# Kernel tuning notes

Hardware: AMD Instinct MI355X
Metric: run time of the kernel (lower is better)

## Reference

```python
import jax, jax.numpy as jnp
import numpy as np

B, S, DIM = 8, 4096, 512
G, V = 2, 320            # num_groups, num_vars
CVD = 256                # codevector_dim
D = CVD // G             # per-group codevector dim = 128
TAU = 2.0                # gumbel temperature


def setup_inputs() -> dict:
    key = jax.random.key(0)
    k1, k2, k3, k4 = jax.random.split(key, 4)
    hidden_states = jax.random.normal(k1, (B, S, DIM), dtype=jnp.float32)
    # weight_proj: Linear(dim -> G*V)
    W = jax.random.normal(k2, (DIM, G * V), dtype=jnp.float32) * 0.02
    b = jnp.zeros((G * V,), dtype=jnp.float32)
    # codebook: torch init is uniform(0,1) on [1, G*V, D]; store as [G*V, D]
    codevectors = jax.random.uniform(k3, (G * V, D), dtype=jnp.float32)
    # standard Gumbel(0,1) noise, one row per (token, group)
    u = jax.random.uniform(k4, (B * S * G, V), dtype=jnp.float32,
                           minval=1e-6, maxval=1.0 - 1e-6)
    gumbels = -jnp.log(-jnp.log(u))
    return {"hidden_states": hidden_states, "W": W, "b": b,
            "codevectors": codevectors, "gumbels": gumbels}


def reference(hidden_states, W, b, codevectors, gumbels):
    Bc, Sc, _ = hidden_states.shape
    T = Bc * Sc
    # weight projection -> logits over codebook entries
    logits = hidden_states @ W + b                      # [B, S, G*V]
    flat = logits.reshape(T * G, V)                     # [T*G, V]

    # gumbel_softmax(hard=True) with straight-through estimator
    y_soft = jax.nn.softmax((flat + gumbels) / TAU, axis=-1)
    hard = jax.nn.one_hot(jnp.argmax(y_soft, axis=-1), V, dtype=y_soft.dtype)
    codevector_probs = hard + y_soft - jax.lax.stop_gradient(y_soft)

    # soft distribution (no gumbel noise, no temperature) per torch code
    codevector_dist = jax.nn.softmax(flat.reshape(T, G, V), axis=-1)

    # one-hot weighted sum over codebook = per-group contraction
    cb = codevectors.reshape(G, V, D)                   # [G, V, D]
    out = jnp.einsum('tgv,gvd->tgd',
                     codevector_probs.reshape(T, G, V), cb)
    out = out.reshape(Bc, Sc, G * D)                    # [B, S, codevector_dim]
    return (out, codevector_dist)
```

## Files before the change

kernel.cpp:

```cpp
#include <hip/hip_runtime.h>

#define Tcnt 32768
#define Gn   2
#define Vn   320
#define Dn   128
#define DIMK 512
#define GV   640
#define RB   64

typedef __attribute__((ext_vector_type(8))) short bf16x8;
typedef __attribute__((ext_vector_type(4))) ushort u16x4;
typedef __attribute__((ext_vector_type(4))) float f32x4;

__device__ inline ushort f2bf(float x) {
    unsigned u = __float_as_uint(x);
    return (ushort)((u + 0x7fffu + ((u >> 16) & 1u)) >> 16);
}

#define AS1(p) ((const __attribute__((address_space(1))) void*)(p))
#define AS3(p) ((__attribute__((address_space(3))) void*)(p))

__global__ __launch_bounds__(256) void prep_wt(
    const float* __restrict__ W, ushort* __restrict__ Wt)
{
    __shared__ ushort Ls[64][72];
    int t = blockIdx.x;
    int n0 = (t % 10) * 64, k0 = (t / 10) * 64;
    int ln = threadIdx.x & 63, kq = threadIdx.x >> 6;
    #pragma unroll
    for (int kk = 0; kk < 16; ++kk) {
        int k = kq * 16 + kk;
        Ls[k][ln] = f2bf(W[(size_t)(k0 + k) * GV + n0 + ln]);
    }
    __syncthreads();
    #pragma unroll
    for (int nn = 0; nn < 16; ++nn) {
        int n = kq * 16 + nn;
        Wt[(size_t)(n0 + n) * DIMK + k0 + ln] = Ls[ln][n];
    }
}

__global__ __launch_bounds__(512, 4) void fused_vq_kernel(
    const float*  __restrict__ hs,
    const ushort* __restrict__ Wt,
    const float*  __restrict__ W,
    const float*  __restrict__ bias,
    const float*  __restrict__ gum,
    const float*  __restrict__ cv,
    float* __restrict__ out,
    float* __restrict__ dist)
{
    __shared__ ushort As[2][RB * 32];
    __shared__ ushort Bs[2][Vn * 32];
    __shared__ float4 part[RB][2];
    __shared__ int    s_cnt[RB];
    __shared__ int    s_col[RB][8];
    __shared__ float  s_s[RB][8];
    __shared__ float  s_gm[RB][8];
    __shared__ int    s_bidx[RB];
    __shared__ float  s_mxs[RB];

    const int tid = threadIdx.x, w = tid >> 6, lane = tid & 63;
    const int Q = lane >> 4, c16 = lane & 15;
    const int wm = (w >> 1) * 16, wn = (w & 1) * 160, half = w & 1;

    const int bid = blockIdx.x;
    const int swz = (bid & 7) * 128 + (bid >> 3);
    const int g = swz & 1;
    const size_t t0 = (size_t)(swz >> 1) * RB;

    if (tid < RB) s_cnt[tid] = 0;

    const int arow_s = tid >> 3, pc = tid & 7;
    const int lq = (pc >> 1) ^ ((arow_s >> 1) & 3);
    const int lc = lq * 2 + (pc & 1);
    const float* asrc = hs + (t0 + arow_s) * DIMK + lc * 4;
    const ushort* wtg = Wt + (size_t)g * Vn * DIMK;

    auto stageB = [&](int buf, int k0) {
        #pragma unroll
        for (int i2 = 0; i2 < 2; ++i2) {
            int s = i2 * 512 + tid;
            int n = s >> 2, pq = s & 3, lqq = pq ^ ((n >> 1) & 3);
            __builtin_amdgcn_global_load_lds(
                AS1(wtg + (size_t)n * DIMK + k0 + lqq * 8),
                AS3(&Bs[buf][s * 8]), 16, 0, 0);
        }
        if (w < 4) {
            int s = 1024 + tid;
            int n = s >> 2, pq = s & 3, lqq = pq ^ ((n >> 1) & 3);
            __builtin_amdgcn_global_load_lds(
                AS1(wtg + (size_t)n * DIMK + k0 + lqq * 8),
                AS3(&Bs[buf][s * 8]), 16, 0, 0);
        }
    };
    auto writeA = [&](int buf, float4 v) {
        u16x4 o;
        o[0] = f2bf(v.x); o[1] = f2bf(v.y); o[2] = f2bf(v.z); o[3] = f2bf(v.w);
        *(u16x4*)&As[buf][tid * 4] = o;
    };

    float4 areg0 = *(const float4*)(asrc);
    stageB(0, 0);
    float4 areg1 = *(const float4*)(asrc + 32);
    writeA(0, areg0);
    __syncthreads();

    f32x4 acc[10];
    #pragma unroll
    for (int j = 0; j < 10; ++j) acc[j] = (f32x4){0.f, 0.f, 0.f, 0.f};

    #pragma unroll
    for (int ks = 0; ks < 16; ++ks) {
        if (ks + 2 < 16) {
            if ((ks & 1) == 0) areg0 = *(const float4*)(asrc + (ks + 2) * 32);
            else               areg1 = *(const float4*)(asrc + (ks + 2) * 32);
        }
        if (ks + 1 < 16) stageB((ks + 1) & 1, (ks + 1) * 32);

        const ushort* Ab = As[ks & 1];
        const ushort* Bb = Bs[ks & 1];
        const int ar = wm + c16;
        bf16x8 af = *(const bf16x8*)&Ab[(ar * 4 + (Q ^ ((ar >> 1) & 3))) * 8];
        #pragma unroll
        for (int j = 0; j < 10; ++j) {
            int n = wn + j * 16 + c16;
            bf16x8 bv = *(const bf16x8*)&Bb[(n * 4 + (Q ^ ((n >> 1) & 3))) * 8];
            acc[j] = __builtin_amdgcn_mfma_f32_16x16x32_bf16(af, bv, acc[j], 0, 0, 0);
        }
        if (ks + 1 < 16) writeA((ks + 1) & 1, ((ks + 1) & 1) ? areg1 : areg0);
        __syncthreads();
    }

    #pragma unroll
    for (int j = 0; j < 10; ++j) {
        float bb = bias[g * Vn + wn + j * 16 + c16];
        acc[j][0] += bb; acc[j][1] += bb; acc[j][2] += bb; acc[j][3] += bb;
    }

    const float MARGIN = 0.0625f;

    #pragma unroll
    for (int qr = 0; qr < 4; ++qr) {
        int row = wm + Q * 4 + qr;
        size_t r2 = (t0 + row) * 2 + g;
        const float* gr = gum + r2 * Vn + wn;
        float sv[10];
        float mxl = -1e30f, mxs = -1e30f; int bi = 0;
        #pragma unroll
        for (int j = 0; j < 10; ++j) {
            float lg = acc[j][qr];
            float gu = gr[j * 16 + c16];
            float s = lg + gu; sv[j] = s;
            mxl = fmaxf(mxl, lg);
            if (s > mxs) { mxs = s; bi = wn + j * 16 + c16; }
        }
        #pragma unroll
        for (int off = 1; off < 16; off <<= 1) {
            mxl = fmaxf(mxl, __shfl_xor(mxl, off));
            float os = __shfl_xor(mxs, off); int ob = __shfl_xor(bi, off);
            if (os > mxs || (os == mxs && ob < bi)) { mxs = os; bi = ob; }
        }
        float sum = 0.f;
        #pragma unroll
        for (int j = 0; j < 10; ++j) sum += __expf(acc[j][qr] - mxl);
        #pragma unroll
        for (int off = 1; off < 16; off <<= 1) sum += __shfl_xor(sum, off);

        float thr = mxs - MARGIN;
        #pragma unroll
        for (int j = 0; j < 10; ++j) {
            if (sv[j] >= thr) {
                int pos = atomicAdd(&s_cnt[row], 1);
                if (pos < 8) {
                    s_col[row][pos] = wn + j * 16 + c16;
                    s_s[row][pos]   = sv[j];
                    s_gm[row][pos]  = sv[j] - acc[j][qr];
                }
            }
        }
        if (c16 == 0)
            part[row][half] = (float4){mxl, sum, mxs, __int_as_float(bi)};
    }
    __syncthreads();

    #pragma unroll
    for (int qr = 0; qr < 4; ++qr) {
        int row = wm + Q * 4 + qr;
        size_t r2 = (t0 + row) * 2 + g;
        float4 mine = part[row][half];
        float4 oth  = part[row][half ^ 1];
        float mxl_f = fmaxf(mine.x, oth.x);
        float sum_f = mine.y * __expf(mine.x - mxl_f) + oth.y * __expf(oth.x - mxl_f);
        float inv = 1.0f / sum_f;
        float* dr = dist + r2 * Vn + wn;
        #pragma unroll
        for (int j = 0; j < 10; ++j)
            dr[j * 16 + c16] = __expf(acc[j][qr] - mxl_f) * inv;
        if (half == 0 && c16 == 0) {
            float ms = mine.z; int mi = __float_as_int(mine.w);
            float os = oth.z;  int oi = __float_as_int(oth.w);
            if (os > ms || (os == ms && oi < mi)) { ms = os; mi = oi; }
            s_mxs[row] = ms; s_bidx[row] = mi;
        }
    }
    __syncthreads();

    for (int ui = 0; ui < 8; ++ui) {
        int u = w * 8 + ui;
        int c = s_cnt[u]; if (c > 8) c = 8;
        float thr = s_mxs[u] - MARGIN;
        int nf = 0;
        for (int j = 0; j < c; ++j) nf += (s_s[u][j] >= thr) ? 1 : 0;
        if (nf > 1) {
            size_t t = t0 + u;
            const float* hr = hs + t * DIMK;
            float4 h0 = *(const float4*)(hr + lane * 8);
            float4 h1 = *(const float4*)(hr + lane * 8 + 4);
            float hv[8] = {h0.x, h0.y, h0.z, h0.w, h1.x, h1.y, h1.z, h1.w};
            float best = -1e30f; int bv2 = 1 << 30;
            for (int j = 0; j < c; ++j) {
                if (s_s[u][j] < thr) continue;
                int v = s_col[u][j];
                int gcol = g * Vn + v;
                const float* wc = W + gcol;
                float p = 0.f;
                #pragma unroll
                for (int i = 0; i < 8; ++i)
                    p = fmaf(hv[i], wc[(size_t)(lane * 8 + i) * GV], p);
                #pragma unroll
                for (int off = 1; off < 64; off <<= 1) p += __shfl_xor(p, off);
                float se = p + bias[gcol] + s_gm[u][j];
                if (se > best || (se == best && v < bv2)) { best = se; bv2 = v; }
            }
            if (lane == 0) s_bidx[u] = bv2;
        }
    }
    __syncthreads();

    for (int ui = 0; ui < 8; ++ui) {
        int u = w * 8 + ui;
        size_t t = t0 + u;
        int b = s_bidx[u];
        const float2* cvr = (const float2*)(cv + ((size_t)(g * Vn + b)) * Dn);
        float2 val = cvr[lane];
        *(float2*)(out + t * (Gn * Dn) + g * Dn + lane * 2) = val;
    }
}

extern "C" void kernel_launch(void* const* d_in, const int* in_sizes, int n_in,
                              void* d_out, int out_size, void* d_ws, size_t ws_size,
                              hipStream_t stream) {
    const float* hs  = (const float*)d_in[0];
    const float* W   = (const float*)d_in[1];
    const float* b   = (const float*)d_in[2];
    const float* cv  = (const float*)d_in[3];
    const float* gum = (const float*)d_in[4];

    float* out  = (float*)d_out;
    float* dist = out + (size_t)Tcnt * (Gn * Dn);
    ushort* Wt  = (ushort*)d_ws;

    prep_wt<<<80, 256, 0, stream>>>(W, Wt);
    fused_vq_kernel<<<(Tcnt / RB) * Gn, 512, 0, stream>>>(hs, Wt, W, b, gum, cv, out, dist);
}
```

Before: 95.80 us.

## Transpose logits through shared memory for row-per-wave softmax and argmax epilogue

Accumulated logits are written to a shared-memory tile (unioned with the GEMM staging buffers) in two halves, so that each wave handles whole rows with lanes spanning the vocabulary. This gives coalesced gumbel loads and dist stores, full-wave reductions, and removes the cross-wave partial-merge pass and its extra barrier. Candidate collection for exact refinement now runs only when more than one column falls inside the margin, which drops the later threshold re-check. The cost is extra LDS traffic plus barriers for the transpose, and a two-phase serialization in which half the waves sit idle while the other half write their tile.

```diff
diff --git a/kernel.cpp b/kernel.cpp
--- a/kernel.cpp
+++ b/kernel.cpp
@@ -50,19 +50,18 @@
     float* __restrict__ out,
     float* __restrict__ dist)
 {
-    __shared__ ushort As[2][RB * 32];
-    __shared__ ushort Bs[2][Vn * 32];
-    __shared__ float4 part[RB][2];
+    __shared__ union SMem {
+        struct { ushort As[2][RB * 32]; ushort Bs[2][Vn * 32]; } gm;
+        float Ls[32][324];
+    } U;
     __shared__ int    s_cnt[RB];
     __shared__ int    s_col[RB][8];
-    __shared__ float  s_s[RB][8];
     __shared__ float  s_gm[RB][8];
     __shared__ int    s_bidx[RB];
-    __shared__ float  s_mxs[RB];
 
     const int tid = threadIdx.x, w = tid >> 6, lane = tid & 63;
     const int Q = lane >> 4, c16 = lane & 15;
-    const int wm = (w >> 1) * 16, wn = (w & 1) * 160, half = w & 1;
+    const int wm = (w >> 1) * 16, wn = (w & 1) * 160;
 
     const int bid = blockIdx.x;
     const int swz = (bid & 7) * 128 + (bid >> 3);
@@ -84,20 +83,20 @@
             int n = s >> 2, pq = s & 3, lqq = pq ^ ((n >> 1) & 3);
             __builtin_amdgcn_global_load_lds(
                 AS1(wtg + (size_t)n * DIMK + k0 + lqq * 8),
-                AS3(&Bs[buf][s * 8]), 16, 0, 0);
+                AS3(&U.gm.Bs[buf][s * 8]), 16, 0, 0);
         }
         if (w < 4) {
             int s = 1024 + tid;
             int n = s >> 2, pq = s & 3, lqq = pq ^ ((n >> 1) & 3);
             __builtin_amdgcn_global_load_lds(
                 AS1(wtg + (size_t)n * DIMK + k0 + lqq * 8),
-                AS3(&Bs[buf][s * 8]), 16, 0, 0);
+                AS3(&U.gm.Bs[buf][s * 8]), 16, 0, 0);
         }
     };
     auto writeA = [&](int buf, float4 v) {
         u16x4 o;
         o[0] = f2bf(v.x); o[1] = f2bf(v.y); o[2] = f2bf(v.z); o[3] = f2bf(v.w);
-        *(u16x4*)&As[buf][tid * 4] = o;
+        *(u16x4*)&U.gm.As[buf][tid * 4] = o;
     };
 
     float4 areg0 = *(const float4*)(asrc);
@@ -118,8 +117,8 @@
         }
         if (ks + 1 < 16) stageB((ks + 1) & 1, (ks + 1) * 32);
 
-        const ushort* Ab = As[ks & 1];
-        const ushort* Bb = Bs[ks & 1];
+        const ushort* Ab = U.gm.As[ks & 1];
+        const ushort* Bb = U.gm.Bs[ks & 1];
         const int ar = wm + c16;
         bf16x8 af = *(const bf16x8*)&Ab[(ar * 4 + (Q ^ ((ar >> 1) & 3))) * 8];
         #pragma unroll
@@ -141,78 +140,78 @@
     const float MARGIN = 0.0625f;
 
     #pragma unroll
-    for (int qr = 0; qr < 4; ++qr) {
-        int row = wm + Q * 4 + qr;
-        size_t r2 = (t0 + row) * 2 + g;
-        const float* gr = gum + r2 * Vn + wn;
-        float sv[10];
-        float mxl = -1e30f, mxs = -1e30f; int bi = 0;
-        #pragma unroll
-        for (int j = 0; j < 10; ++j) {
-            float lg = acc[j][qr];
-            float gu = gr[j * 16 + c16];
-            float s = lg + gu; sv[j] = s;
-            mxl = fmaxf(mxl, lg);
-            if (s > mxs) { mxs = s; bi = wn + j * 16 + c16; }
-        }
-        #pragma unroll
-        for (int off = 1; off < 16; off <<= 1) {
-            mxl = fmaxf(mxl, __shfl_xor(mxl, off));
-            float os = __shfl_xor(mxs, off); int ob = __shfl_xor(bi, off);
-            if (os > mxs || (os == mxs && ob < bi)) { mxs = os; bi = ob; }
-        }
-        float sum = 0.f;
-        #pragma unroll
-        for (int j = 0; j < 10; ++j) sum += __expf(acc[j][qr] - mxl);
-        #pragma unroll
-        for (int off = 1; off < 16; off <<= 1) sum += __shfl_xor(sum, off);
-
-        float thr = mxs - MARGIN;
-        #pragma unroll
-        for (int j = 0; j < 10; ++j) {
-            if (sv[j] >= thr) {
-                int pos = atomicAdd(&s_cnt[row], 1);
-                if (pos < 8) {
-                    s_col[row][pos] = wn + j * 16 + c16;
-                    s_s[row][pos]   = sv[j];
-                    s_gm[row][pos]  = sv[j] - acc[j][qr];
+    for (int grp = 0; grp < 2; ++grp) {
+        __syncthreads();
+        if ((w >> 2) == grp) {
+            #pragma unroll
+            for (int qr = 0; qr < 4; ++qr) {
+                int lrow = (wm - grp * 32) + Q * 4 + qr;
+                #pragma unroll
+                for (int j = 0; j < 10; ++j)
+                    U.Ls[lrow][wn + j * 16 + c16] = acc[j][qr];
+            }
+        }
+        __syncthreads();
+        for (int ri = 0; ri < 4; ++ri) {
+            int rl = w * 4 + ri;
+            int row = grp * 32 + rl;
+            size_t r2 = (t0 + row) * 2 + g;
+            const float* gr = gum + r2 * Vn;
+            float lg[5], sv[5];
+            #pragma unroll
+            for (int j = 0; j < 5; ++j) {
+                lg[j] = U.Ls[rl][lane + j * 64];
+                sv[j] = lg[j] + gr[lane + j * 64];
+            }
+            float mxl = -1e30f, mxs = -1e30f; int bi = 0;
+            #pragma unroll
+            for (int j = 0; j < 5; ++j) {
+                mxl = fmaxf(mxl, lg[j]);
+                if (sv[j] > mxs) { mxs = sv[j]; bi = lane + j * 64; }
+            }
+            #pragma unroll
+            for (int off = 1; off < 64; off <<= 1) {
+                mxl = fmaxf(mxl, __shfl_xor(mxl, off));
+                float os = __shfl_xor(mxs, off); int ob = __shfl_xor(bi, off);
+                if (os > mxs || (os == mxs && ob < bi)) { mxs = os; bi = ob; }
+            }
+            float ev[5]; float sum = 0.f;
+            #pragma unroll
+            for (int j = 0; j < 5; ++j) { ev[j] = __expf(lg[j] - mxl); sum += ev[j]; }
+            #pragma unroll
+            for (int off = 1; off < 64; off <<= 1) sum += __shfl_xor(sum, off);
+            float inv = 1.0f / sum;
+            float* dr = dist + r2 * Vn;
+            #pragma unroll
+            for (int j = 0; j < 5; ++j) dr[lane + j * 64] = ev[j] * inv;
+
+            if (lane == 0) s_bidx[row] = bi;
+            float thr = mxs - MARGIN;
+            int tot = 0;
+            #pragma unroll
+            for (int j = 0; j < 5; ++j)
+                tot += __popcll(__ballot(sv[j] >= thr));
+            if (tot > 1) {
+                #pragma unroll
+                for (int j = 0; j < 5; ++j) {
+                    if (sv[j] >= thr) {
+                        int pos = atomicAdd(&s_cnt[row], 1);
+                        if (pos < 8) {
+                            s_col[row][pos] = lane + j * 64;
+                            s_gm[row][pos]  = sv[j] - lg[j];
+                        }
+                    }
                 }
             }
-        }
-        if (c16 == 0)
-            part[row][half] = (float4){mxl, sum, mxs, __int_as_float(bi)};
-    }
-    __syncthreads();
-
-    #pragma unroll
-    for (int qr = 0; qr < 4; ++qr) {
-        int row = wm + Q * 4 + qr;
-        size_t r2 = (t0 + row) * 2 + g;
-        float4 mine = part[row][half];
-        float4 oth  = part[row][half ^ 1];
-        float mxl_f = fmaxf(mine.x, oth.x);
-        float sum_f = mine.y * __expf(mine.x - mxl_f) + oth.y * __expf(oth.x - mxl_f);
-        float inv = 1.0f / sum_f;
-        float* dr = dist + r2 * Vn + wn;
-        #pragma unroll
-        for (int j = 0; j < 10; ++j)
-            dr[j * 16 + c16] = __expf(acc[j][qr] - mxl_f) * inv;
-        if (half == 0 && c16 == 0) {
-            float ms = mine.z; int mi = __float_as_int(mine.w);
-            float os = oth.z;  int oi = __float_as_int(oth.w);
-            if (os > ms || (os == ms && oi < mi)) { ms = os; mi = oi; }
-            s_mxs[row] = ms; s_bidx[row] = mi;
         }
     }
     __syncthreads();
 
     for (int ui = 0; ui < 8; ++ui) {
         int u = w * 8 + ui;
-        int c = s_cnt[u]; if (c > 8) c = 8;
-        float thr = s_mxs[u] - MARGIN;
-        int nf = 0;
-        for (int j = 0; j < c; ++j) nf += (s_s[u][j] >= thr) ? 1 : 0;
-        if (nf > 1) {
+        int c = s_cnt[u];
+        if (c > 1) {
+            if (c > 8) c = 8;
             size_t t = t0 + u;
             const float* hr = hs + t * DIMK;
             float4 h0 = *(const float4*)(hr + lane * 8);
@@ -220,7 +219,6 @@
             float hv[8] = {h0.x, h0.y, h0.z, h0.w, h1.x, h1.y, h1.z, h1.w};
             float best = -1e30f; int bv2 = 1 << 30;
             for (int j = 0; j < c; ++j) {
-                if (s_s[u][j] < thr) continue;
                 int v = s_col[u][j];
                 int gcol = g * Vn + v;
                 const float* wc = W + gcol;
```

Result: slower. 113.2 us (+18.1%).

## Load GEMM operands directly from global in MFMA fragment layout, drop LDS staging

Applied to the files above, without the earlier changes.

The weight prep kernel now writes W in a pre-swizzled bf16 layout matching the MFMA B-fragment order, so each lane loads its fragment straight from global/L2. A is converted from fp32 to bf16 in registers per wave instead of being staged through double-buffered LDS. The warp tiling changes to 2x4 (32 rows x 80 cols per wave), and the candidate buffer grows to 12. This removes the LDS traffic and per-k-step barriers, but relies on cache hits for repeated W reads and lowers the occupancy hint to 2.

```diff
diff --git a/kernel.cpp b/kernel.cpp
--- a/kernel.cpp
+++ b/kernel.cpp
@@ -1,4 +1,5 @@
 #include <hip/hip_runtime.h>
+#include <hip/hip_bf16.h>
 
 #define Tcnt 32768
 #define Gn   2
@@ -7,42 +8,56 @@
 #define DIMK 512
 #define GV   640
 #define RB   64
+#define NCAND 12
 
 typedef __attribute__((ext_vector_type(8))) short bf16x8;
-typedef __attribute__((ext_vector_type(4))) ushort u16x4;
+typedef __attribute__((ext_vector_type(8))) ushort u16x8;
 typedef __attribute__((ext_vector_type(4))) float f32x4;
 
 __device__ inline ushort f2bf(float x) {
     unsigned u = __float_as_uint(x);
     return (ushort)((u + 0x7fffu + ((u >> 16) & 1u)) >> 16);
 }
-
-#define AS1(p) ((const __attribute__((address_space(1))) void*)(p))
-#define AS3(p) ((__attribute__((address_space(3))) void*)(p))
-
-__global__ __launch_bounds__(256) void prep_wt(
-    const float* __restrict__ W, ushort* __restrict__ Wt)
+__device__ inline ushort nbf(float x) {
+    __hip_bfloat16 h = __float2bfloat16(x);
+    return *reinterpret_cast<ushort*>(&h);
+}
+__device__ inline bf16x8 cvt8(float4 a, float4 b) {
+    u16x8 o;
+    o[0]=nbf(a.x); o[1]=nbf(a.y); o[2]=nbf(a.z); o[3]=nbf(a.w);
+    o[4]=nbf(b.x); o[5]=nbf(b.y); o[6]=nbf(b.z); o[7]=nbf(b.w);
+    return (bf16x8)o;
+}
+
+__global__ __launch_bounds__(256) void prep_wt2(
+    const float* __restrict__ W, ushort* __restrict__ Wt2)
 {
-    __shared__ ushort Ls[64][72];
-    int t = blockIdx.x;
-    int n0 = (t % 10) * 64, k0 = (t / 10) * 64;
-    int ln = threadIdx.x & 63, kq = threadIdx.x >> 6;
-    #pragma unroll
-    for (int kk = 0; kk < 16; ++kk) {
-        int k = kq * 16 + kk;
-        Ls[k][ln] = f2bf(W[(size_t)(k0 + k) * GV + n0 + ln]);
-    }
-    __syncthreads();
-    #pragma unroll
-    for (int nn = 0; nn < 16; ++nn) {
-        int n = kq * 16 + nn;
-        Wt[(size_t)(n0 + n) * DIMK + k0 + ln] = Ls[ln][n];
-    }
-}
-
-__global__ __launch_bounds__(512, 4) void fused_vq_kernel(
+    __shared__ ushort Ls[512][17];
+    const int gnb = blockIdx.x;
+    const int colbase = gnb * 16;
+    const int t = threadIdx.x;
+    const int c = t & 15, kq = t >> 4;
+    for (int r = 0; r < 32; ++r) {
+        int k = r * 16 + kq;
+        Ls[k][c] = f2bf(W[(size_t)k * GV + colbase + c]);
+    }
+    __syncthreads();
+    #pragma unroll
+    for (int ii = 0; ii < 4; ++ii) {
+        int ls = ii * 256 + t;
+        int ks = ls >> 6, lane = ls & 63;
+        int c16 = lane & 15, Q = lane >> 4;
+        u16x8 o;
+        #pragma unroll
+        for (int s = 0; s < 8; ++s)
+            o[s] = Ls[ks * 32 + Q * 8 + s][c16];
+        *(u16x8*)(Wt2 + (((size_t)gnb * 16 + ks) * 64 + lane) * 8) = o;
+    }
+}
+
+__global__ __launch_bounds__(512, 2) void fused_vq_kernel(
     const float*  __restrict__ hs,
-    const ushort* __restrict__ Wt,
+    const ushort* __restrict__ Wt2,
     const float*  __restrict__ W,
     const float*  __restrict__ bias,
     const float*  __restrict__ gum,
@@ -50,19 +65,19 @@
     float* __restrict__ out,
     float* __restrict__ dist)
 {
-    __shared__ ushort As[2][RB * 32];
-    __shared__ ushort Bs[2][Vn * 32];
-    __shared__ float4 part[RB][2];
+    __shared__ float4 part[RB][4];
     __shared__ int    s_cnt[RB];
-    __shared__ int    s_col[RB][8];
-    __shared__ float  s_s[RB][8];
-    __shared__ float  s_gm[RB][8];
+    __shared__ int    s_col[RB][NCAND];
+    __shared__ float  s_s[RB][NCAND];
+    __shared__ float  s_gm[RB][NCAND];
     __shared__ int    s_bidx[RB];
     __shared__ float  s_mxs[RB];
 
     const int tid = threadIdx.x, w = tid >> 6, lane = tid & 63;
     const int Q = lane >> 4, c16 = lane & 15;
-    const int wm = (w >> 1) * 16, wn = (w & 1) * 160, half = w & 1;
+    const int wrow = (w >> 2) * 32;
+    const int wq = w & 3;
+    const int wn = wq * 80;
 
     const int bid = blockIdx.x;
     const int swz = (bid & 7) * 128 + (bid >> 3);
@@ -71,40 +86,9 @@
 
     if (tid < RB) s_cnt[tid] = 0;
 
-    const int arow_s = tid >> 3, pc = tid & 7;
-    const int lq = (pc >> 1) ^ ((arow_s >> 1) & 3);
-    const int lc = lq * 2 + (pc & 1);
-    const float* asrc = hs + (t0 + arow_s) * DIMK + lc * 4;
-    const ushort* wtg = Wt + (size_t)g * Vn * DIMK;
-
-    auto stageB = [&](int buf, int k0) {
-        #pragma unroll
-        for (int i2 = 0; i2 < 2; ++i2) {
-            int s = i2 * 512 + tid;
-            int n = s >> 2, pq = s & 3, lqq = pq ^ ((n >> 1) & 3);
-            __builtin_amdgcn_global_load_lds(
-                AS1(wtg + (size_t)n * DIMK + k0 + lqq * 8),
-                AS3(&Bs[buf][s * 8]), 16, 0, 0);
-        }
-        if (w < 4) {
-            int s = 1024 + tid;
-            int n = s >> 2, pq = s & 3, lqq = pq ^ ((n >> 1) & 3);
-            __builtin_amdgcn_global_load_lds(
-                AS1(wtg + (size_t)n * DIMK + k0 + lqq * 8),
-                AS3(&Bs[buf][s * 8]), 16, 0, 0);
-        }
-    };
-    auto writeA = [&](int buf, float4 v) {
-        u16x4 o;
-        o[0] = f2bf(v.x); o[1] = f2bf(v.y); o[2] = f2bf(v.z); o[3] = f2bf(v.w);
-        *(u16x4*)&As[buf][tid * 4] = o;
-    };
-
-    float4 areg0 = *(const float4*)(asrc);
-    stageB(0, 0);
-    float4 areg1 = *(const float4*)(asrc + 32);
-    writeA(0, areg0);
-    __syncthreads();
+    const float* a0p = hs + (t0 + wrow + c16) * DIMK + Q * 8;
+    const float* a1p = a0p + 16 * DIMK;
+    const ushort* bb = Wt2 + ((size_t)(g * 20 + wq * 5) * 16 * 64) * 8 + lane * 8;
 
     f32x4 acc[10];
     #pragma unroll
@@ -112,48 +96,46 @@
 
     #pragma unroll
     for (int ks = 0; ks < 16; ++ks) {
-        if (ks + 2 < 16) {
-            if ((ks & 1) == 0) areg0 = *(const float4*)(asrc + (ks + 2) * 32);
-            else               areg1 = *(const float4*)(asrc + (ks + 2) * 32);
-        }
-        if (ks + 1 < 16) stageB((ks + 1) & 1, (ks + 1) * 32);
-
-        const ushort* Ab = As[ks & 1];
-        const ushort* Bb = Bs[ks & 1];
-        const int ar = wm + c16;
-        bf16x8 af = *(const bf16x8*)&Ab[(ar * 4 + (Q ^ ((ar >> 1) & 3))) * 8];
-        #pragma unroll
-        for (int j = 0; j < 10; ++j) {
-            int n = wn + j * 16 + c16;
-            bf16x8 bv = *(const bf16x8*)&Bb[(n * 4 + (Q ^ ((n >> 1) & 3))) * 8];
-            acc[j] = __builtin_amdgcn_mfma_f32_16x16x32_bf16(af, bv, acc[j], 0, 0, 0);
-        }
-        if (ks + 1 < 16) writeA((ks + 1) & 1, ((ks + 1) & 1) ? areg1 : areg0);
-        __syncthreads();
-    }
-
-    #pragma unroll
-    for (int j = 0; j < 10; ++j) {
-        float bb = bias[g * Vn + wn + j * 16 + c16];
-        acc[j][0] += bb; acc[j][1] += bb; acc[j][2] += bb; acc[j][3] += bb;
-    }
+        float4 x0 = *(const float4*)(a0p + ks * 32);
+        float4 x1 = *(const float4*)(a0p + ks * 32 + 4);
+        float4 y0 = *(const float4*)(a1p + ks * 32);
+        float4 y1 = *(const float4*)(a1p + ks * 32 + 4);
+        bf16x8 af0 = cvt8(x0, x1);
+        bf16x8 af1 = cvt8(y0, y1);
+        #pragma unroll
+        for (int j = 0; j < 5; ++j) {
+            bf16x8 bv = *(const bf16x8*)(bb + ((size_t)j * 16 + ks) * 512);
+            acc[j]     = __builtin_amdgcn_mfma_f32_16x16x32_bf16(af0, bv, acc[j],     0, 0, 0);
+            acc[5 + j] = __builtin_amdgcn_mfma_f32_16x16x32_bf16(af1, bv, acc[5 + j], 0, 0, 0);
+        }
+    }
+
+    #pragma unroll
+    for (int j = 0; j < 5; ++j) {
+        float bbv = bias[g * Vn + wn + j * 16 + c16];
+        #pragma unroll
+        for (int qq = 0; qq < 4; ++qq) { acc[j][qq] += bbv; acc[5 + j][qq] += bbv; }
+    }
+
+    __syncthreads();
 
     const float MARGIN = 0.0625f;
 
     #pragma unroll
-    for (int qr = 0; qr < 4; ++qr) {
-        int row = wm + Q * 4 + qr;
+    for (int i = 0; i < 2; ++i) {
+      #pragma unroll
+      for (int qr = 0; qr < 4; ++qr) {
+        int row = wrow + i * 16 + Q * 4 + qr;
         size_t r2 = (t0 + row) * 2 + g;
         const float* gr = gum + r2 * Vn + wn;
-        float sv[10];
+        float lg[5], sv[5];
         float mxl = -1e30f, mxs = -1e30f; int bi = 0;
         #pragma unroll
-        for (int j = 0; j < 10; ++j) {
-            float lg = acc[j][qr];
-            float gu = gr[j * 16 + c16];
-            float s = lg + gu; sv[j] = s;
-            mxl = fmaxf(mxl, lg);
-            if (s > mxs) { mxs = s; bi = wn + j * 16 + c16; }
+        for (int j = 0; j < 5; ++j) {
+            lg[j] = acc[i * 5 + j][qr];
+            sv[j] = lg[j] + gr[j * 16 + c16];
+            mxl = fmaxf(mxl, lg[j]);
+            if (sv[j] > mxs) { mxs = sv[j]; bi = wn + j * 16 + c16; }
         }
         #pragma unroll
         for (int off = 1; off < 16; off <<= 1) {
@@ -163,52 +145,56 @@
         }
         float sum = 0.f;
         #pragma unroll
-        for (int j = 0; j < 10; ++j) sum += __expf(acc[j][qr] - mxl);
+        for (int j = 0; j < 5; ++j) sum += __expf(lg[j] - mxl);
         #pragma unroll
         for (int off = 1; off < 16; off <<= 1) sum += __shfl_xor(sum, off);
 
         float thr = mxs - MARGIN;
         #pragma unroll
-        for (int j = 0; j < 10; ++j) {
+        for (int j = 0; j < 5; ++j) {
             if (sv[j] >= thr) {
                 int pos = atomicAdd(&s_cnt[row], 1);
-                if (pos < 8) {
+                if (pos < NCAND) {
                     s_col[row][pos] = wn + j * 16 + c16;
                     s_s[row][pos]   = sv[j];
-                    s_gm[row][pos]  = sv[j] - acc[j][qr];
+                    s_gm[row][pos]  = sv[j] - lg[j];
                 }
             }
         }
-        if (c16 == 0)
-            part[row][half] = (float4){mxl, sum, mxs, __int_as_float(bi)};
-    }
-    __syncthreads();
-
-    #pragma unroll
-    for (int qr = 0; qr < 4; ++qr) {
-        int row = wm + Q * 4 + qr;
+        if (c16 == 0) part[row][wq] = (float4){mxl, sum, mxs, __int_as_float(bi)};
+      }
+    }
+    __syncthreads();
+
+    #pragma unroll
+    for (int i = 0; i < 2; ++i) {
+      #pragma unroll
+      for (int qr = 0; qr < 4; ++qr) {
+        int row = wrow + i * 16 + Q * 4 + qr;
         size_t r2 = (t0 + row) * 2 + g;
-        float4 mine = part[row][half];
-        float4 oth  = part[row][half ^ 1];
-        float mxl_f = fmaxf(mine.x, oth.x);
-        float sum_f = mine.y * __expf(mine.x - mxl_f) + oth.y * __expf(oth.x - mxl_f);
+        float4 p0 = part[row][0], p1 = part[row][1], p2 = part[row][2], p3 = part[row][3];
+        float mxl_f = fmaxf(fmaxf(p0.x, p1.x), fmaxf(p2.x, p3.x));
+        float sum_f = p0.y * __expf(p0.x - mxl_f) + p1.y * __expf(p1.x - mxl_f)
+                    + p2.y * __expf(p2.x - mxl_f) + p3.y * __expf(p3.x - mxl_f);
         float inv = 1.0f / sum_f;
         float* dr = dist + r2 * Vn + wn;
         #pragma unroll
-        for (int j = 0; j < 10; ++j)
-            dr[j * 16 + c16] = __expf(acc[j][qr] - mxl_f) * inv;
-        if (half == 0 && c16 == 0) {
-            float ms = mine.z; int mi = __float_as_int(mine.w);
-            float os = oth.z;  int oi = __float_as_int(oth.w);
-            if (os > ms || (os == ms && oi < mi)) { ms = os; mi = oi; }
+        for (int j = 0; j < 5; ++j)
+            dr[j * 16 + c16] = __expf(acc[i * 5 + j][qr] - mxl_f) * inv;
+        if (wq == 0 && c16 == 0) {
+            float ms = p0.z; int mi = __float_as_int(p0.w);
+            if (p1.z > ms || (p1.z == ms && __float_as_int(p1.w) < mi)) { ms = p1.z; mi = __float_as_int(p1.w); }
+            if (p2.z > ms || (p2.z == ms && __float_as_int(p2.w) < mi)) { ms = p2.z; mi = __float_as_int(p2.w); }
+            if (p3.z > ms || (p3.z == ms && __float_as_int(p3.w) < mi)) { ms = p3.z; mi = __float_as_int(p3.w); }
             s_mxs[row] = ms; s_bidx[row] = mi;
         }
+      }
     }
     __syncthreads();
 
     for (int ui = 0; ui < 8; ++ui) {
         int u = w * 8 + ui;
-        int c = s_cnt[u]; if (c > 8) c = 8;
+        int c = s_cnt[u]; if (c > NCAND) c = NCAND;
         float thr = s_mxs[u] - MARGIN;
         int nf = 0;
         for (int j = 0; j < c; ++j) nf += (s_s[u][j] >= thr) ? 1 : 0;
@@ -226,8 +212,8 @@
                 const float* wc = W + gcol;
                 float p = 0.f;
                 #pragma unroll
-                for (int i = 0; i < 8; ++i)
-                    p = fmaf(hv[i], wc[(size_t)(lane * 8 + i) * GV], p);
+                for (int i2 = 0; i2 < 8; ++i2)
+                    p = fmaf(hv[i2], wc[(size_t)(lane * 8 + i2) * GV], p);
                 #pragma unroll
                 for (int off = 1; off < 64; off <<= 1) p += __shfl_xor(p, off);
                 float se = p + bias[gcol] + s_gm[u][j];
@@ -241,8 +227,8 @@
     for (int ui = 0; ui < 8; ++ui) {
         int u = w * 8 + ui;
         size_t t = t0 + u;
-        int b = s_bidx[u];
-        const float2* cvr = (const float2*)(cv + ((size_t)(g * Vn + b)) * Dn);
+        int b2 = s_bidx[u];
+        const float2* cvr = (const float2*)(cv + ((size_t)(g * Vn + b2)) * Dn);
         float2 val = cvr[lane];
         *(float2*)(out + t * (Gn * Dn) + g * Dn + lane * 2) = val;
     }
@@ -259,8 +245,8 @@
 
     float* out  = (float*)d_out;
     float* dist = out + (size_t)Tcnt * (Gn * Dn);
-    ushort* Wt  = (ushort*)d_ws;
-
-    prep_wt<<<80, 256, 0, stream>>>(W, Wt);
-    fused_vq_kernel<<<(Tcnt / RB) * Gn, 512, 0, stream>>>(hs, Wt, W, b, gum, cv, out, dist);
-}
+    ushort* Wt2 = (ushort*)d_ws;
+
+    prep_wt2<<<40, 256, 0, stream>>>(W, Wt2);
+    fused_vq_kernel<<<(Tcnt / RB) * Gn, 512, 0, stream>>>(hs, Wt2, W, b, gum, cv, out, dist);
+}
```

Measured after the change: 194.0 us. +102.5%, slower.

## Double row tile to 128 with 1024-thread blocks and union LDS buffers

Applied to the files above, without the earlier changes.

Raises the row block from 64 to 128 tokens and the block size to 1024 threads, so each staged B tile of projection weights is reused across twice as many rows. The GEMM staging buffers and the epilogue scratch arrays now share one LDS union, which keeps the larger tile's shared memory footprint down. An extra barrier is added before the counter reset because the two regions overlap. The cost is fewer, larger blocks (512 in total) and possibly lower occupancy given the launch_bounds of (1024,4) and the per-thread register usage.

```diff
diff --git a/kernel.cpp b/kernel.cpp
--- a/kernel.cpp
+++ b/kernel.cpp
@@ -6,7 +6,8 @@
 #define Dn   128
 #define DIMK 512
 #define GV   640
-#define RB   64
+#define RB   128
+#define NCAND 8
 
 typedef __attribute__((ext_vector_type(8))) short bf16x8;
 typedef __attribute__((ext_vector_type(4))) ushort u16x4;
@@ -40,7 +41,7 @@
     }
 }
 
-__global__ __launch_bounds__(512, 4) void fused_vq_kernel(
+__global__ __launch_bounds__(1024, 4) void fused_vq_kernel(
     const float*  __restrict__ hs,
     const ushort* __restrict__ Wt,
     const float*  __restrict__ W,
@@ -50,26 +51,28 @@
     float* __restrict__ out,
     float* __restrict__ dist)
 {
-    __shared__ ushort As[2][RB * 32];
-    __shared__ ushort Bs[2][Vn * 32];
-    __shared__ float4 part[RB][2];
-    __shared__ int    s_cnt[RB];
-    __shared__ int    s_col[RB][8];
-    __shared__ float  s_s[RB][8];
-    __shared__ float  s_gm[RB][8];
-    __shared__ int    s_bidx[RB];
-    __shared__ float  s_mxs[RB];
+    union SMem {
+        struct { ushort As[2][RB * 32]; ushort Bs[2][Vn * 32]; } gm;
+        struct {
+            float4 part[RB][2];
+            int    cnt[RB];
+            int    col[RB][NCAND];
+            float  sc[RB][NCAND];
+            float  gmv[RB][NCAND];
+            int    bidx[RB];
+            float  mxs[RB];
+        } ep;
+    };
+    __shared__ SMem U;
 
     const int tid = threadIdx.x, w = tid >> 6, lane = tid & 63;
     const int Q = lane >> 4, c16 = lane & 15;
     const int wm = (w >> 1) * 16, wn = (w & 1) * 160, half = w & 1;
 
     const int bid = blockIdx.x;
-    const int swz = (bid & 7) * 128 + (bid >> 3);
+    const int swz = (bid & 7) * 64 + (bid >> 3);
     const int g = swz & 1;
     const size_t t0 = (size_t)(swz >> 1) * RB;
-
-    if (tid < RB) s_cnt[tid] = 0;
 
     const int arow_s = tid >> 3, pc = tid & 7;
     const int lq = (pc >> 1) ^ ((arow_s >> 1) & 3);
@@ -78,26 +81,25 @@
     const ushort* wtg = Wt + (size_t)g * Vn * DIMK;
 
     auto stageB = [&](int buf, int k0) {
-        #pragma unroll
-        for (int i2 = 0; i2 < 2; ++i2) {
-            int s = i2 * 512 + tid;
+        {
+            int s = tid;
             int n = s >> 2, pq = s & 3, lqq = pq ^ ((n >> 1) & 3);
             __builtin_amdgcn_global_load_lds(
                 AS1(wtg + (size_t)n * DIMK + k0 + lqq * 8),
-                AS3(&Bs[buf][s * 8]), 16, 0, 0);
-        }
-        if (w < 4) {
+                AS3(&U.gm.Bs[buf][s * 8]), 16, 0, 0);
+        }
+        if (tid < 256) {
             int s = 1024 + tid;
             int n = s >> 2, pq = s & 3, lqq = pq ^ ((n >> 1) & 3);
             __builtin_amdgcn_global_load_lds(
                 AS1(wtg + (size_t)n * DIMK + k0 + lqq * 8),
-                AS3(&Bs[buf][s * 8]), 16, 0, 0);
+                AS3(&U.gm.Bs[buf][s * 8]), 16, 0, 0);
         }
     };
     auto writeA = [&](int buf, float4 v) {
         u16x4 o;
         o[0] = f2bf(v.x); o[1] = f2bf(v.y); o[2] = f2bf(v.z); o[3] = f2bf(v.w);
-        *(u16x4*)&As[buf][tid * 4] = o;
+        *(u16x4*)&U.gm.As[buf][tid * 4] = o;
     };
 
     float4 areg0 = *(const float4*)(asrc);
@@ -118,8 +120,8 @@
         }
         if (ks + 1 < 16) stageB((ks + 1) & 1, (ks + 1) * 32);
 
-        const ushort* Ab = As[ks & 1];
-        const ushort* Bb = Bs[ks & 1];
+        const ushort* Ab = U.gm.As[ks & 1];
+        const ushort* Bb = U.gm.Bs[ks & 1];
         const int ar = wm + c16;
         bf16x8 af = *(const bf16x8*)&Ab[(ar * 4 + (Q ^ ((ar >> 1) & 3))) * 8];
         #pragma unroll
@@ -137,6 +139,9 @@
         float bb = bias[g * Vn + wn + j * 16 + c16];
         acc[j][0] += bb; acc[j][1] += bb; acc[j][2] += bb; acc[j][3] += bb;
     }
+
+    if (tid < RB) U.ep.cnt[tid] = 0;
+    __syncthreads();
 
     const float MARGIN = 0.0625f;
 
@@ -171,16 +176,16 @@
         #pragma unroll
         for (int j = 0; j < 10; ++j) {
             if (sv[j] >= thr) {
-                int pos = atomicAdd(&s_cnt[row], 1);
-                if (pos < 8) {
-                    s_col[row][pos] = wn + j * 16 + c16;
-                    s_s[row][pos]   = sv[j];
-                    s_gm[row][pos]  = sv[j] - acc[j][qr];
+                int pos = atomicAdd(&U.ep.cnt[row], 1);
+                if (pos < NCAND) {
+                    U.ep.col[row][pos] = wn + j * 16 + c16;
+                    U.ep.sc[row][pos]  = sv[j];
+                    U.ep.gmv[row][pos] = sv[j] - acc[j][qr];
                 }
             }
         }
         if (c16 == 0)
-            part[row][half] = (float4){mxl, sum, mxs, __int_as_float(bi)};
+            U.ep.part[row][half] = (float4){mxl, sum, mxs, __int_as_float(bi)};
     }
     __syncthreads();
 
@@ -188,8 +193,8 @@
     for (int qr = 0; qr < 4; ++qr) {
         int row = wm + Q * 4 + qr;
         size_t r2 = (t0 + row) * 2 + g;
-        float4 mine = part[row][half];
-        float4 oth  = part[row][half ^ 1];
+        float4 mine = U.ep.part[row][half];
+        float4 oth  = U.ep.part[row][half ^ 1];
         float mxl_f = fmaxf(mine.x, oth.x);
         float sum_f = mine.y * __expf(mine.x - mxl_f) + oth.y * __expf(oth.x - mxl_f);
         float inv = 1.0f / sum_f;
@@ -201,17 +206,17 @@
             float ms = mine.z; int mi = __float_as_int(mine.w);
             float os = oth.z;  int oi = __float_as_int(oth.w);
             if (os > ms || (os == ms && oi < mi)) { ms = os; mi = oi; }
-            s_mxs[row] = ms; s_bidx[row] = mi;
+            U.ep.mxs[row] = ms; U.ep.bidx[row] = mi;
         }
     }
     __syncthreads();
 
     for (int ui = 0; ui < 8; ++ui) {
         int u = w * 8 + ui;
-        int c = s_cnt[u]; if (c > 8) c = 8;
-        float thr = s_mxs[u] - MARGIN;
+        int c = U.ep.cnt[u]; if (c > NCAND) c = NCAND;
+        float thr = U.ep.mxs[u] - MARGIN;
         int nf = 0;
-        for (int j = 0; j < c; ++j) nf += (s_s[u][j] >= thr) ? 1 : 0;
+        for (int j = 0; j < c; ++j) nf += (U.ep.sc[u][j] >= thr) ? 1 : 0;
         if (nf > 1) {
             size_t t = t0 + u;
             const float* hr = hs + t * DIMK;
@@ -220,8 +225,8 @@
             float hv[8] = {h0.x, h0.y, h0.z, h0.w, h1.x, h1.y, h1.z, h1.w};
             float best = -1e30f; int bv2 = 1 << 30;
             for (int j = 0; j < c; ++j) {
-                if (s_s[u][j] < thr) continue;
-                int v = s_col[u][j];
+                if (U.ep.sc[u][j] < thr) continue;
+                int v = U.ep.col[u][j];
                 int gcol = g * Vn + v;
                 const float* wc = W + gcol;
                 float p = 0.f;
@@ -230,10 +235,10 @@
                     p = fmaf(hv[i], wc[(size_t)(lane * 8 + i) * GV], p);
                 #pragma unroll
                 for (int off = 1; off < 64; off <<= 1) p += __shfl_xor(p, off);
-                float se = p + bias[gcol] + s_gm[u][j];
+                float se = p + bias[gcol] + U.ep.gmv[u][j];
                 if (se > best || (se == best && v < bv2)) { best = se; bv2 = v; }
             }
-            if (lane == 0) s_bidx[u] = bv2;
+            if (lane == 0) U.ep.bidx[u] = bv2;
         }
     }
     __syncthreads();
@@ -241,7 +246,7 @@
     for (int ui = 0; ui < 8; ++ui) {
         int u = w * 8 + ui;
         size_t t = t0 + u;
-        int b = s_bidx[u];
+        int b = U.ep.bidx[u];
         const float2* cvr = (const float2*)(cv + ((size_t)(g * Vn + b)) * Dn);
         float2 val = cvr[lane];
         *(float2*)(out + t * (Gn * Dn) + g * Dn + lane * 2) = val;
@@ -262,5 +267,5 @@
     ushort* Wt  = (ushort*)d_ws;
 
     prep_wt<<<80, 256, 0, stream>>>(W, Wt);
-    fused_vq_kernel<<<(Tcnt / RB) * Gn, 512, 0, stream>>>(hs, Wt, W, b, gum, cv, out, dist);
-}
+    fused_vq_kernel<<<(Tcnt / RB) * Gn, 1024, 0, stream>>>(hs, Wt, W, b, gum, cv, out, dist);
+}
```

After: 92.33 us. 3.6% less time.
